# Optimization experiments

Hardware: AMD Instinct MI355X
Metric: run time of the kernel (lower is better)

## Reference

```python
import jax, jax.numpy as jnp
import numpy as np

N_NODES = 20000
N_EDGES = 320000
BATCH = 8
N_OBS = 6
N_FIXED = 10
HID = 128
N_LAYERS = 3


def setup_inputs() -> dict:
    key = jax.random.key(0)
    ks = jax.random.split(key, 6)
    x = jax.random.normal(ks[0], (BATCH * N_NODES, N_OBS), dtype=jnp.float32)
    fixed_node_features = jax.random.normal(ks[1], (N_NODES, N_FIXED), dtype=jnp.float32)
    edge_index = jax.random.randint(ks[2], (2, N_EDGES), 0, N_NODES)
    W_in = jax.random.normal(ks[3], (N_OBS + N_FIXED, HID), dtype=jnp.float32) * 0.1
    b_in = jnp.zeros((HID,), jnp.float32)
    Wg = jax.random.normal(ks[4], (N_LAYERS, HID, HID), dtype=jnp.float32) * 0.05
    bg = jnp.zeros((N_LAYERS, HID), jnp.float32)
    return {"x": x, "fixed_node_features": fixed_node_features, "W_in": W_in,
            "b_in": b_in, "Wg": Wg, "bg": bg, "edge_index": edge_index}


def reference(x, fixed_node_features, W_in, b_in, Wg, bg, edge_index):
    # GCN normalization with self-loops (PyG gcn_norm defaults):
    self_loops = jnp.arange(N_NODES)
    row = jnp.concatenate([edge_index[0], self_loops])  # source nodes [E+N]
    col = jnp.concatenate([edge_index[1], self_loops])  # target nodes [E+N]
    deg = jax.ops.segment_sum(jnp.ones_like(col, dtype=jnp.float32), col,
                              num_segments=N_NODES)
    dinv = jnp.where(deg > 0, jax.lax.rsqrt(jnp.maximum(deg, 1.0)), 0.0)
    norm = dinv[row] * dinv[col]  # [E+N]

    # input projection: [B*N, n_obs] -> [B, N, n_obs+n_fixed] -> [B, N, H]
    h = x.reshape(BATCH, N_NODES, N_OBS)
    h = jnp.concatenate(
        [h, jnp.broadcast_to(fixed_node_features, (BATCH, N_NODES, N_FIXED))],
        axis=-1)
    h = h @ W_in + b_in

    # stacked GCNConv + ReLU (gather -> normalize -> scatter-add)
    for l in range(N_LAYERS):
        t = h @ Wg[l]                              # [B, N, H]
        msgs = t[:, row, :] * norm[None, :, None]  # [B, E+N, H]
        agg = jnp.zeros_like(t).at[:, col, :].add(msgs)
        h = jax.nn.relu(agg + bg[l])

    return h.reshape(-1, HID)
```

## Files before the change

### kernel.cpp

```cpp
#include <hip/hip_runtime.h>
#include <hip/hip_bf16.h>
#include <cstdint>

#define N_NODES 20000
#define N_EDGES 320000
#define BATCH 8
#define HID 128

static constexpr size_t O_DEG  = 0;
static constexpr size_t O_CUR  = 81920;
static constexpr size_t O_OFF  = 163840;
static constexpr size_t O_DINV = 245760;
static constexpr size_t O_CSR  = 327680;
static constexpr size_t O_HBUF = 2891776;


__global__ void count_deg(const int* __restrict__ col, int* __restrict__ deg) {
    int e = blockIdx.x * 256 + threadIdx.x;
    if (e < N_EDGES) atomicAdd(&deg[col[e]], 1);
}

__global__ void compute_dinv(const int* __restrict__ deg, float* __restrict__ dinv) {
    int i = blockIdx.x * 256 + threadIdx.x;
    if (i < N_NODES) {
        float d = (float)(deg[i] + 1);
        dinv[i] = 1.0f / sqrtf(d);
    }
}

__global__ __launch_bounds__(1024) void scan_offsets(const int* __restrict__ deg,
                                                     int* __restrict__ off) {
    __shared__ int part[1024];
    const int CH = 20;
    int tid = threadIdx.x;
    int base = tid * CH;
    int s = 0;
    for (int i = 0; i < CH; ++i) {
        int idx = base + i;
        if (idx < N_NODES) s += deg[idx];
    }
    part[tid] = s;
    __syncthreads();
    for (int d = 1; d < 1024; d <<= 1) {
        int add = 0;
        if (tid >= d) add = part[tid - d];
        __syncthreads();
        part[tid] += add;
        __syncthreads();
    }
    int run = part[tid] - s;
    for (int i = 0; i < CH; ++i) {
        int idx = base + i;
        if (idx < N_NODES) {
            off[idx] = run;
            run += deg[idx];
        }
    }
    if (tid == 1023) off[N_NODES] = part[1023];
}

__global__ void fill_csr(const int* __restrict__ rowi, const int* __restrict__ coli,
                         const int* __restrict__ off, int* __restrict__ cursor,
                         uint16_t* __restrict__ csr) {
    int e = blockIdx.x * 256 + threadIdx.x;
    if (e >= N_EDGES) return;
    int r = rowi[e], c = coli[e];
    int pos = atomicAdd(&cursor[c], 1);
    csr[off[c] + pos] = (uint16_t)r;
}

__global__ __launch_bounds__(64) void sort_adj(const int* __restrict__ off,
                                               uint16_t* __restrict__ csr) {
    int n = blockIdx.x;
    int s = off[n], e = off[n + 1];
    int deg = e - s;
    if (deg <= 1 || deg > 64) return;
    int l = threadIdx.x;
    int my = (l < deg) ? (int)csr[s + l] : 0x7fffffff;
    int rank = 0;
    for (int j = 0; j < deg; ++j) {
        int kj = __shfl(my, j);
        rank += (kj < my) || (kj == my && j < l);
    }
    if (l < deg) csr[s + rank] = (uint16_t)my;
}

__global__ __launch_bounds__(256) void input_proj(const float* __restrict__ x,
                                                  const float* __restrict__ fixedf,
                                                  const float* __restrict__ W,
                                                  const float* __restrict__ bvec,
                                                  float* __restrict__ h) {
    __shared__ float Ws[16 * HID];
    __shared__ float xs[BATCH * 6];
    __shared__ float fs[10];
    int n = blockIdx.x, tid = threadIdx.x;
    for (int i = tid; i < 16 * HID; i += 256) Ws[i] = W[i];
    if (tid < 48) {
        int b_ = tid / 6, o = tid % 6;
        xs[tid] = x[((size_t)b_ * N_NODES + n) * 6 + o];
    } else if (tid < 58) {
        fs[tid - 48] = fixedf[(size_t)n * 10 + (tid - 48)];
    }
    __syncthreads();
#pragma unroll
    for (int j = 0; j < 4; ++j) {
        int idx = tid + j * 256;
        int bb = idx >> 7, hh = idx & 127;
        float acc = bvec[hh];
#pragma unroll
        for (int k = 0; k < 6; ++k) acc += xs[bb * 6 + k] * Ws[k * HID + hh];
#pragma unroll
        for (int k = 0; k < 10; ++k) acc += fs[k] * Ws[(6 + k) * HID + hh];
        size_t a = ((size_t)((hh >> 5) * 8 + bb) * N_NODES + n) * 32 + (hh & 31);
        h[a] = acc;
    }
}

__global__ __launch_bounds__(256) void aggregate_xcd(const float* __restrict__ hin,
                                                     const int* __restrict__ off,
                                                     const uint16_t* __restrict__ csr,
                                                     const float* __restrict__ dinv,
                                                     float* __restrict__ out,
                                                     int final_scatter) {
    int bid = blockIdx.x;
    int b   = bid & 7;
    int q   = bid / 5000;
    int g   = (bid - q * 5000) >> 3;
    int tid = threadIdx.x;
    int l = tid & 63;
    int n = g * 32 + ((tid >> 6) << 3) + (l >> 3);
    int sub = l & 7;
    const size_t SB4 = (size_t)(q * 8 + b) * N_NODES * 8;

    const float4* hp4 = (const float4*)hin;
    float dn = dinv[n];
    float d2 = dn * dn;
    float4 acc = hp4[SB4 + (size_t)n * 8 + sub];
    acc.x *= d2; acc.y *= d2; acc.z *= d2; acc.w *= d2;

    int s = off[n], e = off[n + 1];
    int p = s;
    for (; p + 2 <= e; p += 2) {
        int s0 = csr[p], s1 = csr[p + 1];
        float w0 = dinv[s0] * dn, w1 = dinv[s1] * dn;
        float4 v0 = hp4[SB4 + (size_t)s0 * 8 + sub];
        float4 v1 = hp4[SB4 + (size_t)s1 * 8 + sub];
        acc.x += w0 * v0.x + w1 * v1.x;
        acc.y += w0 * v0.y + w1 * v1.y;
        acc.z += w0 * v0.z + w1 * v1.z;
        acc.w += w0 * v0.w + w1 * v1.w;
    }
    if (p < e) {
        int s0 = csr[p];
        float w0 = dinv[s0] * dn;
        float4 v0 = hp4[SB4 + (size_t)s0 * 8 + sub];
        acc.x += w0 * v0.x; acc.y += w0 * v0.y;
        acc.z += w0 * v0.z; acc.w += w0 * v0.w;
    }

    size_t o4 = final_scatter ? ((size_t)(b * N_NODES + n) * 32 + q * 8 + sub)
                              : (SB4 + (size_t)n * 8 + sub);
    ((float4*)out)[o4] = acc;
}

__global__ __launch_bounds__(256) void gemm_bias_relu(const float* __restrict__ in,
                                                      float* __restrict__ outp,
                                                      const float* __restrict__ W,
                                                      const float* __restrict__ bias,
                                                      int dense) {
    __shared__ float As_T[32][132];
    __shared__ float Wls[32][HID];
    int tid = threadIdx.x;
    int rg = tid >> 4;
    int cg = tid & 15;
    int b  = blockIdx.x / 157;
    int n0 = (blockIdx.x % 157) * 128;
    float acc[8][8] = {};
    const float4* in4 = (const float4*)in;

    for (int kt = 0; kt < HID; kt += 32) {
        int q = kt >> 5;
        __syncthreads();
#pragma unroll
        for (int i = 0; i < 4; ++i) {
            int f = tid + i * 256;
            int row = f >> 3;
            int kk4 = f & 7;
            int n = n0 + row;
            if (n > N_NODES - 1) n = N_NODES - 1;
            size_t rb4 = dense ? (((size_t)b * N_NODES + n) * 32 + q * 8)
                               : (((size_t)(q * 8 + b) * N_NODES + n) * 8);
            float4 v = in4[rb4 + kk4];
            int kk = kk4 << 2;
            As_T[kk + 0][row] = v.x;
            As_T[kk + 1][row] = v.y;
            As_T[kk + 2][row] = v.z;
            As_T[kk + 3][row] = v.w;
        }
#pragma unroll
        for (int i = 0; i < 4; ++i) {
            int f = tid + i * 256;
            int row = f >> 5;
            int kk = (f & 31) << 2;
            *(float4*)&Wls[row][kk] = *(const float4*)&W[(size_t)(kt + row) * HID + kk];
        }
        __syncthreads();
#pragma unroll 8
        for (int k = 0; k < 32; ++k) {
            float4 a0 = *(const float4*)&As_T[k][rg * 8];
            float4 a1 = *(const float4*)&As_T[k][rg * 8 + 4];
            float4 w0 = *(const float4*)&Wls[k][cg * 4];
            float4 w1 = *(const float4*)&Wls[k][cg * 4 + 64];
            float av[8] = {a0.x, a0.y, a0.z, a0.w, a1.x, a1.y, a1.z, a1.w};
            float wv[8] = {w0.x, w0.y, w0.z, w0.w, w1.x, w1.y, w1.z, w1.w};
#pragma unroll
            for (int i = 0; i < 8; ++i)
#pragma unroll
                for (int j = 0; j < 8; ++j)
                    acc[i][j] += av[i] * wv[j];
        }
    }

    float4 b0 = *(const float4*)&bias[cg * 4];
    float4 b1 = *(const float4*)&bias[cg * 4 + 64];
    float4* out4 = (float4*)outp;
#pragma unroll
    for (int i = 0; i < 8; ++i) {
        int n = n0 + rg * 8 + i;
        if (n >= N_NODES) break;
        float4 o0, o1;
        o0.x = fmaxf(acc[i][0] + b0.x, 0.0f);
        o0.y = fmaxf(acc[i][1] + b0.y, 0.0f);
        o0.z = fmaxf(acc[i][2] + b0.z, 0.0f);
        o0.w = fmaxf(acc[i][3] + b0.w, 0.0f);
        o1.x = fmaxf(acc[i][4] + b1.x, 0.0f);
        o1.y = fmaxf(acc[i][5] + b1.y, 0.0f);
        o1.z = fmaxf(acc[i][6] + b1.z, 0.0f);
        o1.w = fmaxf(acc[i][7] + b1.w, 0.0f);
        if (dense) {
            size_t r4 = ((size_t)b * N_NODES + n) * 32;
            out4[r4 + cg] = o0;
            out4[r4 + cg + 16] = o1;
        } else {
            int q0 = cg >> 3, f0 = cg & 7;
            out4[((size_t)(q0 * 8 + b) * N_NODES + n) * 8 + f0] = o0;
            out4[((size_t)((q0 + 2) * 8 + b) * N_NODES + n) * 8 + f0] = o1;
        }
    }
}

extern "C" void kernel_launch(void* const* d_in, const int* in_sizes, int n_in,
                              void* d_out, int out_size, void* d_ws, size_t ws_size,
                              hipStream_t stream) {
    const float* x      = (const float*)d_in[0];
    const float* fixedf = (const float*)d_in[1];
    const float* W_in   = (const float*)d_in[2];
    const float* b_in   = (const float*)d_in[3];
    const float* Wg     = (const float*)d_in[4];
    const float* bg     = (const float*)d_in[5];
    const int*   ei     = (const int*)d_in[6];

    const int* rowi = ei;
    const int* coli = ei + N_EDGES;

    char* ws = (char*)d_ws;
    int*      deg    = (int*)(ws + O_DEG);
    int*      cursor = (int*)(ws + O_CUR);
    int*      off    = (int*)(ws + O_OFF);
    float*    dinv   = (float*)(ws + O_DINV);
    uint16_t* csr    = (uint16_t*)(ws + O_CSR);
    float*    hA     = (float*)(ws + O_HBUF);
    float*    hB     = (float*)d_out;

    hipMemsetAsync(deg, 0, N_NODES * sizeof(int), stream);
    hipMemsetAsync(cursor, 0, N_NODES * sizeof(int), stream);

    count_deg<<<(N_EDGES + 255) / 256, 256, 0, stream>>>(coli, deg);
    compute_dinv<<<(N_NODES + 255) / 256, 256, 0, stream>>>(deg, dinv);
    scan_offsets<<<1, 1024, 0, stream>>>(deg, off);
    fill_csr<<<(N_EDGES + 255) / 256, 256, 0, stream>>>(rowi, coli, off, cursor, csr);
    sort_adj<<<N_NODES, 64, 0, stream>>>(off, csr);

    input_proj<<<N_NODES, 256, 0, stream>>>(x, fixedf, W_in, b_in, hA);

    const int AB = 4 * 5000;
    const int GB = 8 * 157;

    aggregate_xcd<<<AB, 256, 0, stream>>>(hA, off, csr, dinv, hB, 0);
    gemm_bias_relu<<<GB, 256, 0, stream>>>(hB, hB, Wg + 0 * HID * HID, bg + 0 * HID, 0);
    aggregate_xcd<<<AB, 256, 0, stream>>>(hB, off, csr, dinv, hA, 0);
    gemm_bias_relu<<<GB, 256, 0, stream>>>(hA, hA, Wg + 1 * HID * HID, bg + 1 * HID, 0);
    aggregate_xcd<<<AB, 256, 0, stream>>>(hA, off, csr, dinv, (float*)d_out, 1);
    gemm_bias_relu<<<GB, 256, 0, stream>>>((float*)d_out, (float*)d_out,
                                           Wg + 2 * HID * HID, bg + 2 * HID, 1);
}
```

Before: 637.9 us.

## Precompute per-edge GCN weights and enlarge GEMM tile to 256 rows

fill_csr now stores each edge's normalized weight dinv[r]*dinv[c] next to the CSR index, and sort_adj permutes those weights along with the indices. The aggregation kernel reads these weights sequentially instead of gathering dinv for every neighbor, and unrolls the neighbor loop by 4 with two accumulators to keep more loads in flight. The dense GEMM tile grows to 256 nodes per block with an 8x16 per-thread accumulator, giving each block more reuse of the staged weights. The costs are an extra 1.28 MB weight array to build and read, and higher register and LDS use in the GEMM, which may lower occupancy.

```diff
diff --git a/kernel.cpp b/kernel.cpp
--- a/kernel.cpp
+++ b/kernel.cpp
@@ -12,6 +12,7 @@
 static constexpr size_t O_OFF  = 163840;
 static constexpr size_t O_DINV = 245760;
 static constexpr size_t O_CSR  = 327680;
+static constexpr size_t O_CSRW = 967680;
 static constexpr size_t O_HBUF = 2891776;
 
 
@@ -60,29 +61,34 @@
 }
 
 __global__ void fill_csr(const int* __restrict__ rowi, const int* __restrict__ coli,
-                         const int* __restrict__ off, int* __restrict__ cursor,
-                         uint16_t* __restrict__ csr) {
+                         const float* __restrict__ dinv, const int* __restrict__ off,
+                         int* __restrict__ cursor, uint16_t* __restrict__ csr,
+                         float* __restrict__ csrw) {
     int e = blockIdx.x * 256 + threadIdx.x;
     if (e >= N_EDGES) return;
     int r = rowi[e], c = coli[e];
     int pos = atomicAdd(&cursor[c], 1);
-    csr[off[c] + pos] = (uint16_t)r;
+    int i = off[c] + pos;
+    csr[i] = (uint16_t)r;
+    csrw[i] = dinv[r] * dinv[c];
 }
 
 __global__ __launch_bounds__(64) void sort_adj(const int* __restrict__ off,
-                                               uint16_t* __restrict__ csr) {
+                                               uint16_t* __restrict__ csr,
+                                               float* __restrict__ csrw) {
     int n = blockIdx.x;
     int s = off[n], e = off[n + 1];
     int deg = e - s;
     if (deg <= 1 || deg > 64) return;
     int l = threadIdx.x;
     int my = (l < deg) ? (int)csr[s + l] : 0x7fffffff;
+    float mw = (l < deg) ? csrw[s + l] : 0.0f;
     int rank = 0;
     for (int j = 0; j < deg; ++j) {
         int kj = __shfl(my, j);
         rank += (kj < my) || (kj == my && j < l);
     }
-    if (l < deg) csr[s + rank] = (uint16_t)my;
+    if (l < deg) { csr[s + rank] = (uint16_t)my; csrw[s + rank] = mw; }
 }
 
 __global__ __launch_bounds__(256) void input_proj(const float* __restrict__ x,
@@ -119,6 +125,7 @@
 __global__ __launch_bounds__(256) void aggregate_xcd(const float* __restrict__ hin,
                                                      const int* __restrict__ off,
                                                      const uint16_t* __restrict__ csr,
+                                                     const float* __restrict__ csrw,
                                                      const float* __restrict__ dinv,
                                                      float* __restrict__ out,
                                                      int final_scatter) {
@@ -137,52 +144,56 @@
     float d2 = dn * dn;
     float4 acc = hp4[SB4 + (size_t)n * 8 + sub];
     acc.x *= d2; acc.y *= d2; acc.z *= d2; acc.w *= d2;
+    float4 acc2 = make_float4(0.f, 0.f, 0.f, 0.f);
 
     int s = off[n], e = off[n + 1];
     int p = s;
-    for (; p + 2 <= e; p += 2) {
-        int s0 = csr[p], s1 = csr[p + 1];
-        float w0 = dinv[s0] * dn, w1 = dinv[s1] * dn;
+    for (; p + 4 <= e; p += 4) {
+        int s0 = csr[p], s1 = csr[p + 1], s2 = csr[p + 2], s3 = csr[p + 3];
+        float w0 = csrw[p], w1 = csrw[p + 1], w2 = csrw[p + 2], w3 = csrw[p + 3];
         float4 v0 = hp4[SB4 + (size_t)s0 * 8 + sub];
         float4 v1 = hp4[SB4 + (size_t)s1 * 8 + sub];
-        acc.x += w0 * v0.x + w1 * v1.x;
-        acc.y += w0 * v0.y + w1 * v1.y;
-        acc.z += w0 * v0.z + w1 * v1.z;
-        acc.w += w0 * v0.w + w1 * v1.w;
-    }
-    if (p < e) {
+        float4 v2 = hp4[SB4 + (size_t)s2 * 8 + sub];
+        float4 v3 = hp4[SB4 + (size_t)s3 * 8 + sub];
+        acc.x += w0 * v0.x + w1 * v1.x;  acc2.x += w2 * v2.x + w3 * v3.x;
+        acc.y += w0 * v0.y + w1 * v1.y;  acc2.y += w2 * v2.y + w3 * v3.y;
+        acc.z += w0 * v0.z + w1 * v1.z;  acc2.z += w2 * v2.z + w3 * v3.z;
+        acc.w += w0 * v0.w + w1 * v1.w;  acc2.w += w2 * v2.w + w3 * v3.w;
+    }
+    for (; p < e; ++p) {
         int s0 = csr[p];
-        float w0 = dinv[s0] * dn;
+        float w0 = csrw[p];
         float4 v0 = hp4[SB4 + (size_t)s0 * 8 + sub];
         acc.x += w0 * v0.x; acc.y += w0 * v0.y;
         acc.z += w0 * v0.z; acc.w += w0 * v0.w;
     }
+    acc.x += acc2.x; acc.y += acc2.y; acc.z += acc2.z; acc.w += acc2.w;
 
     size_t o4 = final_scatter ? ((size_t)(b * N_NODES + n) * 32 + q * 8 + sub)
                               : (SB4 + (size_t)n * 8 + sub);
     ((float4*)out)[o4] = acc;
 }
 
-__global__ __launch_bounds__(256) void gemm_bias_relu(const float* __restrict__ in,
-                                                      float* __restrict__ outp,
-                                                      const float* __restrict__ W,
-                                                      const float* __restrict__ bias,
-                                                      int dense) {
-    __shared__ float As_T[32][132];
-    __shared__ float Wls[32][HID];
+__global__ void gemm_bias_relu(const float* __restrict__ in,
+                               float* __restrict__ outp,
+                               const float* __restrict__ W,
+                               const float* __restrict__ bias,
+                               int dense) {
+    __shared__ float As_T[32][264];
+    __shared__ float Wls[32][132];
     int tid = threadIdx.x;
-    int rg = tid >> 4;
-    int cg = tid & 15;
-    int b  = blockIdx.x / 157;
-    int n0 = (blockIdx.x % 157) * 128;
-    float acc[8][8] = {};
+    int rg = tid >> 3;
+    int cg = tid & 7;
+    int b  = blockIdx.x / 79;
+    int n0 = (blockIdx.x % 79) * 256;
+    float acc[8][16] = {};
     const float4* in4 = (const float4*)in;
 
     for (int kt = 0; kt < HID; kt += 32) {
         int q = kt >> 5;
         __syncthreads();
 #pragma unroll
-        for (int i = 0; i < 4; ++i) {
+        for (int i = 0; i < 8; ++i) {
             int f = tid + i * 256;
             int row = f >> 3;
             int kk4 = f & 7;
@@ -205,46 +216,44 @@
             *(float4*)&Wls[row][kk] = *(const float4*)&W[(size_t)(kt + row) * HID + kk];
         }
         __syncthreads();
-#pragma unroll 8
+#pragma unroll 2
         for (int k = 0; k < 32; ++k) {
             float4 a0 = *(const float4*)&As_T[k][rg * 8];
             float4 a1 = *(const float4*)&As_T[k][rg * 8 + 4];
-            float4 w0 = *(const float4*)&Wls[k][cg * 4];
-            float4 w1 = *(const float4*)&Wls[k][cg * 4 + 64];
             float av[8] = {a0.x, a0.y, a0.z, a0.w, a1.x, a1.y, a1.z, a1.w};
-            float wv[8] = {w0.x, w0.y, w0.z, w0.w, w1.x, w1.y, w1.z, w1.w};
-#pragma unroll
-            for (int i = 0; i < 8; ++i)
-#pragma unroll
-                for (int j = 0; j < 8; ++j)
-                    acc[i][j] += av[i] * wv[j];
-        }
-    }
-
-    float4 b0 = *(const float4*)&bias[cg * 4];
-    float4 b1 = *(const float4*)&bias[cg * 4 + 64];
+#pragma unroll
+            for (int m = 0; m < 4; ++m) {
+                float4 w4 = *(const float4*)&Wls[k][cg * 4 + m * 32];
+                float wv[4] = {w4.x, w4.y, w4.z, w4.w};
+#pragma unroll
+                for (int i = 0; i < 8; ++i)
+#pragma unroll
+                    for (int j = 0; j < 4; ++j)
+                        acc[i][m * 4 + j] += av[i] * wv[j];
+            }
+        }
+    }
+
     float4* out4 = (float4*)outp;
 #pragma unroll
-    for (int i = 0; i < 8; ++i) {
-        int n = n0 + rg * 8 + i;
-        if (n >= N_NODES) break;
-        float4 o0, o1;
-        o0.x = fmaxf(acc[i][0] + b0.x, 0.0f);
-        o0.y = fmaxf(acc[i][1] + b0.y, 0.0f);
-        o0.z = fmaxf(acc[i][2] + b0.z, 0.0f);
-        o0.w = fmaxf(acc[i][3] + b0.w, 0.0f);
-        o1.x = fmaxf(acc[i][4] + b1.x, 0.0f);
-        o1.y = fmaxf(acc[i][5] + b1.y, 0.0f);
-        o1.z = fmaxf(acc[i][6] + b1.z, 0.0f);
-        o1.w = fmaxf(acc[i][7] + b1.w, 0.0f);
-        if (dense) {
-            size_t r4 = ((size_t)b * N_NODES + n) * 32;
-            out4[r4 + cg] = o0;
-            out4[r4 + cg + 16] = o1;
-        } else {
-            int q0 = cg >> 3, f0 = cg & 7;
-            out4[((size_t)(q0 * 8 + b) * N_NODES + n) * 8 + f0] = o0;
-            out4[((size_t)((q0 + 2) * 8 + b) * N_NODES + n) * 8 + f0] = o1;
+    for (int m = 0; m < 4; ++m) {
+        int col = cg * 4 + m * 32;
+        float4 bb = *(const float4*)&bias[col];
+#pragma unroll
+        for (int i = 0; i < 8; ++i) {
+            int n = n0 + rg * 8 + i;
+            if (n >= N_NODES) break;
+            float4 o;
+            o.x = fmaxf(acc[i][m * 4 + 0] + bb.x, 0.0f);
+            o.y = fmaxf(acc[i][m * 4 + 1] + bb.y, 0.0f);
+            o.z = fmaxf(acc[i][m * 4 + 2] + bb.z, 0.0f);
+            o.w = fmaxf(acc[i][m * 4 + 3] + bb.w, 0.0f);
+            if (dense) {
+                out4[((size_t)b * N_NODES + n) * 32 + (col >> 2)] = o;
+            } else {
+                int q0 = col >> 5, f0 = (col & 31) >> 2;
+                out4[((size_t)(q0 * 8 + b) * N_NODES + n) * 8 + f0] = o;
+            }
         }
     }
 }
@@ -269,6 +278,7 @@
     int*      off    = (int*)(ws + O_OFF);
     float*    dinv   = (float*)(ws + O_DINV);
     uint16_t* csr    = (uint16_t*)(ws + O_CSR);
+    float*    csrw   = (float*)(ws + O_CSRW);
     float*    hA     = (float*)(ws + O_HBUF);
     float*    hB     = (float*)d_out;
 
@@ -278,19 +288,20 @@
     count_deg<<<(N_EDGES + 255) / 256, 256, 0, stream>>>(coli, deg);
     compute_dinv<<<(N_NODES + 255) / 256, 256, 0, stream>>>(deg, dinv);
     scan_offsets<<<1, 1024, 0, stream>>>(deg, off);
-    fill_csr<<<(N_EDGES + 255) / 256, 256, 0, stream>>>(rowi, coli, off, cursor, csr);
-    sort_adj<<<N_NODES, 64, 0, stream>>>(off, csr);
+    fill_csr<<<(N_EDGES + 255) / 256, 256, 0, stream>>>(rowi, coli, dinv, off, cursor,
+                                                        csr, csrw);
+    sort_adj<<<N_NODES, 64, 0, stream>>>(off, csr, csrw);
 
     input_proj<<<N_NODES, 256, 0, stream>>>(x, fixedf, W_in, b_in, hA);
 
     const int AB = 4 * 5000;
-    const int GB = 8 * 157;
-
-    aggregate_xcd<<<AB, 256, 0, stream>>>(hA, off, csr, dinv, hB, 0);
+    const int GB = 8 * 79;
+
+    aggregate_xcd<<<AB, 256, 0, stream>>>(hA, off, csr, csrw, dinv, hB, 0);
     gemm_bias_relu<<<GB, 256, 0, stream>>>(hB, hB, Wg + 0 * HID * HID, bg + 0 * HID, 0);
-    aggregate_xcd<<<AB, 256, 0, stream>>>(hB, off, csr, dinv, hA, 0);
+    aggregate_xcd<<<AB, 256, 0, stream>>>(hB, off, csr, csrw, dinv, hA, 0);
     gemm_bias_relu<<<GB, 256, 0, stream>>>(hA, hA, Wg + 1 * HID * HID, bg + 1 * HID, 0);
-    aggregate_xcd<<<AB, 256, 0, stream>>>(hA, off, csr, dinv, (float*)d_out, 1);
+    aggregate_xcd<<<AB, 256, 0, stream>>>(hA, off, csr, csrw, dinv, (float*)d_out, 1);
     gemm_bias_relu<<<GB, 256, 0, stream>>>((float*)d_out, (float*)d_out,
                                            Wg + 2 * HID * HID, bg + 2 * HID, 1);
 }
```

Result: slower. 2.190 ms (+243.3%).

## Pad CSR rows to multiples of eight with precomputed edge weights

Applied to the files above, without the earlier changes.

Each node's adjacency list is padded to a multiple of eight entries, and edge normalization weights are precomputed into a parallel float array during CSR construction. The aggregation loop then reads eight indices and eight weights with vector loads and issues eight independent gathers per iteration, split across two accumulators. This removes the per-edge dinv lookup and the tail handling, and exposes more memory-level parallelism. The cost is up to seven padding edges per node, which are extra gathers with zero weight, plus a weight array that must be read alongside the indices.

```diff
diff --git a/kernel.cpp b/kernel.cpp
--- a/kernel.cpp
+++ b/kernel.cpp
@@ -12,7 +12,8 @@
 static constexpr size_t O_OFF  = 163840;
 static constexpr size_t O_DINV = 245760;
 static constexpr size_t O_CSR  = 327680;
-static constexpr size_t O_HBUF = 2891776;
+static constexpr size_t O_CSRW = 1376256;
+static constexpr size_t O_HBUF = 3473408;
 
 
 __global__ void count_deg(const int* __restrict__ col, int* __restrict__ deg) {
@@ -37,7 +38,7 @@
     int s = 0;
     for (int i = 0; i < CH; ++i) {
         int idx = base + i;
-        if (idx < N_NODES) s += deg[idx];
+        if (idx < N_NODES) s += (deg[idx] + 7) & ~7;
     }
     part[tid] = s;
     __syncthreads();
@@ -53,36 +54,56 @@
         int idx = base + i;
         if (idx < N_NODES) {
             off[idx] = run;
-            run += deg[idx];
+            run += (deg[idx] + 7) & ~7;
         }
     }
     if (tid == 1023) off[N_NODES] = part[1023];
 }
 
 __global__ void fill_csr(const int* __restrict__ rowi, const int* __restrict__ coli,
-                         const int* __restrict__ off, int* __restrict__ cursor,
-                         uint16_t* __restrict__ csr) {
+                         const float* __restrict__ dinv, const int* __restrict__ off,
+                         int* __restrict__ cursor, uint16_t* __restrict__ csr,
+                         float* __restrict__ csrw) {
     int e = blockIdx.x * 256 + threadIdx.x;
     if (e >= N_EDGES) return;
     int r = rowi[e], c = coli[e];
     int pos = atomicAdd(&cursor[c], 1);
-    csr[off[c] + pos] = (uint16_t)r;
-}
-
-__global__ __launch_bounds__(64) void sort_adj(const int* __restrict__ off,
-                                               uint16_t* __restrict__ csr) {
+    int i = off[c] + pos;
+    csr[i] = (uint16_t)r;
+    csrw[i] = dinv[r] * dinv[c];
+}
+
+__global__ void pad_csr(const int* __restrict__ deg, const int* __restrict__ off,
+                        uint16_t* __restrict__ csr, float* __restrict__ csrw) {
+    int n = blockIdx.x * 256 + threadIdx.x;
+    if (n >= N_NODES) return;
+    int d = deg[n];
+    int pd = (d + 7) & ~7;
+    int s = off[n];
+    uint16_t filler = d > 0 ? csr[s + d - 1] : (uint16_t)n;
+    for (int i = d; i < pd; ++i) {
+        csr[s + i] = filler;
+        csrw[s + i] = 0.0f;
+    }
+}
+
+__global__ __launch_bounds__(64) void sort_adj(const int* __restrict__ degv,
+                                               const int* __restrict__ off,
+                                               uint16_t* __restrict__ csr,
+                                               float* __restrict__ csrw) {
     int n = blockIdx.x;
-    int s = off[n], e = off[n + 1];
-    int deg = e - s;
+    int s = off[n];
+    int deg = degv[n];
     if (deg <= 1 || deg > 64) return;
     int l = threadIdx.x;
     int my = (l < deg) ? (int)csr[s + l] : 0x7fffffff;
+    float mw = (l < deg) ? csrw[s + l] : 0.0f;
     int rank = 0;
     for (int j = 0; j < deg; ++j) {
         int kj = __shfl(my, j);
         rank += (kj < my) || (kj == my && j < l);
     }
-    if (l < deg) csr[s + rank] = (uint16_t)my;
+    if (l < deg) { csr[s + rank] = (uint16_t)my; csrw[s + rank] = mw; }
 }
 
 __global__ __launch_bounds__(256) void input_proj(const float* __restrict__ x,
@@ -119,6 +140,7 @@
 __global__ __launch_bounds__(256) void aggregate_xcd(const float* __restrict__ hin,
                                                      const int* __restrict__ off,
                                                      const uint16_t* __restrict__ csr,
+                                                     const float* __restrict__ csrw,
                                                      const float* __restrict__ dinv,
                                                      float* __restrict__ out,
                                                      int final_scatter) {
@@ -137,26 +159,35 @@
     float d2 = dn * dn;
     float4 acc = hp4[SB4 + (size_t)n * 8 + sub];
     acc.x *= d2; acc.y *= d2; acc.z *= d2; acc.w *= d2;
-
-    int s = off[n], e = off[n + 1];
-    int p = s;
-    for (; p + 2 <= e; p += 2) {
-        int s0 = csr[p], s1 = csr[p + 1];
-        float w0 = dinv[s0] * dn, w1 = dinv[s1] * dn;
+    float4 acc2 = make_float4(0.f, 0.f, 0.f, 0.f);
+
+    int s = off[n], e = s + (off[n + 1] - s);
+    for (int p = s; p < e; p += 8) {
+        uint4  iv = *(const uint4*)(csr + p);
+        float4 wa = *(const float4*)(csrw + p);
+        float4 wb = *(const float4*)(csrw + p + 4);
+        int s0 = iv.x & 0xffff, s1 = iv.x >> 16;
+        int s2 = iv.y & 0xffff, s3 = iv.y >> 16;
+        int s4 = iv.z & 0xffff, s5 = iv.z >> 16;
+        int s6 = iv.w & 0xffff, s7 = iv.w >> 16;
         float4 v0 = hp4[SB4 + (size_t)s0 * 8 + sub];
         float4 v1 = hp4[SB4 + (size_t)s1 * 8 + sub];
-        acc.x += w0 * v0.x + w1 * v1.x;
-        acc.y += w0 * v0.y + w1 * v1.y;
-        acc.z += w0 * v0.z + w1 * v1.z;
-        acc.w += w0 * v0.w + w1 * v1.w;
-    }
-    if (p < e) {
-        int s0 = csr[p];
-        float w0 = dinv[s0] * dn;
-        float4 v0 = hp4[SB4 + (size_t)s0 * 8 + sub];
-        acc.x += w0 * v0.x; acc.y += w0 * v0.y;
-        acc.z += w0 * v0.z; acc.w += w0 * v0.w;
-    }
+        float4 v2 = hp4[SB4 + (size_t)s2 * 8 + sub];
+        float4 v3 = hp4[SB4 + (size_t)s3 * 8 + sub];
+        float4 v4 = hp4[SB4 + (size_t)s4 * 8 + sub];
+        float4 v5 = hp4[SB4 + (size_t)s5 * 8 + sub];
+        float4 v6 = hp4[SB4 + (size_t)s6 * 8 + sub];
+        float4 v7 = hp4[SB4 + (size_t)s7 * 8 + sub];
+        acc.x  += wa.x * v0.x + wa.y * v1.x + wa.z * v2.x + wa.w * v3.x;
+        acc.y  += wa.x * v0.y + wa.y * v1.y + wa.z * v2.y + wa.w * v3.y;
+        acc.z  += wa.x * v0.z + wa.y * v1.z + wa.z * v2.z + wa.w * v3.z;
+        acc.w  += wa.x * v0.w + wa.y * v1.w + wa.z * v2.w + wa.w * v3.w;
+        acc2.x += wb.x * v4.x + wb.y * v5.x + wb.z * v6.x + wb.w * v7.x;
+        acc2.y += wb.x * v4.y + wb.y * v5.y + wb.z * v6.y + wb.w * v7.y;
+        acc2.z += wb.x * v4.z + wb.y * v5.z + wb.z * v6.z + wb.w * v7.z;
+        acc2.w += wb.x * v4.w + wb.y * v5.w + wb.z * v6.w + wb.w * v7.w;
+    }
+    acc.x += acc2.x; acc.y += acc2.y; acc.z += acc2.z; acc.w += acc2.w;
 
     size_t o4 = final_scatter ? ((size_t)(b * N_NODES + n) * 32 + q * 8 + sub)
                               : (SB4 + (size_t)n * 8 + sub);
@@ -269,6 +300,7 @@
     int*      off    = (int*)(ws + O_OFF);
     float*    dinv   = (float*)(ws + O_DINV);
     uint16_t* csr    = (uint16_t*)(ws + O_CSR);
+    float*    csrw   = (float*)(ws + O_CSRW);
     float*    hA     = (float*)(ws + O_HBUF);
     float*    hB     = (float*)d_out;
 
@@ -278,19 +310,21 @@
     count_deg<<<(N_EDGES + 255) / 256, 256, 0, stream>>>(coli, deg);
     compute_dinv<<<(N_NODES + 255) / 256, 256, 0, stream>>>(deg, dinv);
     scan_offsets<<<1, 1024, 0, stream>>>(deg, off);
-    fill_csr<<<(N_EDGES + 255) / 256, 256, 0, stream>>>(rowi, coli, off, cursor, csr);
-    sort_adj<<<N_NODES, 64, 0, stream>>>(off, csr);
+    fill_csr<<<(N_EDGES + 255) / 256, 256, 0, stream>>>(rowi, coli, dinv, off, cursor,
+                                                        csr, csrw);
+    pad_csr<<<(N_NODES + 255) / 256, 256, 0, stream>>>(deg, off, csr, csrw);
+    sort_adj<<<N_NODES, 64, 0, stream>>>(deg, off, csr, csrw);
 
     input_proj<<<N_NODES, 256, 0, stream>>>(x, fixedf, W_in, b_in, hA);
 
     const int AB = 4 * 5000;
     const int GB = 8 * 157;
 
-    aggregate_xcd<<<AB, 256, 0, stream>>>(hA, off, csr, dinv, hB, 0);
+    aggregate_xcd<<<AB, 256, 0, stream>>>(hA, off, csr, csrw, dinv, hB, 0);
     gemm_bias_relu<<<GB, 256, 0, stream>>>(hB, hB, Wg + 0 * HID * HID, bg + 0 * HID, 0);
-    aggregate_xcd<<<AB, 256, 0, stream>>>(hB, off, csr, dinv, hA, 0);
+    aggregate_xcd<<<AB, 256, 0, stream>>>(hB, off, csr, csrw, dinv, hA, 0);
     gemm_bias_relu<<<GB, 256, 0, stream>>>(hA, hA, Wg + 1 * HID * HID, bg + 1 * HID, 0);
-    aggregate_xcd<<<AB, 256, 0, stream>>>(hA, off, csr, dinv, (float*)d_out, 1);
+    aggregate_xcd<<<AB, 256, 0, stream>>>(hA, off, csr, csrw, dinv, (float*)d_out, 1);
     gemm_bias_relu<<<GB, 256, 0, stream>>>((float*)d_out, (float*)d_out,
                                            Wg + 2 * HID * HID, bg + 2 * HID, 1);
 }
```

Result: faster. 591.7 us (-7.2%).
